# Performance work log

Measured on AMD Instinct MI355X. Metric: run time of the kernel, lower is better.

The kernel has to match this reference:

```python
import jax, jax.numpy as jnp
import numpy as np

F_SIZE = 256
N_HEAD = 4
D_HEAD = F_SIZE // N_HEAD
B = 16384
E = 31  # number of 'other' entities


def setup_inputs() -> dict:
    key = jax.random.key(0)
    ks = jax.random.split(key, 9)
    s = 1.0 / np.sqrt(F_SIZE)  # ~ nn.Linear init scale
    inp = {
        "ego": jax.random.normal(ks[0], (B, 1, F_SIZE), dtype=jnp.float32),
        "others": jax.random.normal(ks[1], (B, E, F_SIZE), dtype=jnp.float32),
        "mask": jax.random.randint(ks[2], (B, E + 1), 0, 2).astype(bool),
        "Wq": jax.random.uniform(ks[3], (F_SIZE, F_SIZE), jnp.float32, -s, s),
        "Wk": jax.random.uniform(ks[4], (F_SIZE, F_SIZE), jnp.float32, -s, s),
        "Wv": jax.random.uniform(ks[5], (F_SIZE, F_SIZE), jnp.float32, -s, s),
        "Wok": jax.random.uniform(ks[6], (F_SIZE, F_SIZE), jnp.float32, -s, s),
        "Wov": jax.random.uniform(ks[7], (F_SIZE, F_SIZE), jnp.float32, -s, s),
        "Wc": jax.random.uniform(ks[8], (F_SIZE, F_SIZE), jnp.float32, -s, s),
    }
    return inp


def reference(ego, others, mask, Wq, Wk, Wv, Wok, Wov, Wc):
    b = others.shape[0]
    e = others.shape[1]
    # nn.Linear(bias=False): y = x @ W.T
    ego_q = (ego @ Wq.T).reshape(b, 1, N_HEAD, D_HEAD)
    ego_k = (ego @ Wk.T).reshape(b, 1, N_HEAD, D_HEAD)
    ego_v = (ego @ Wv.T).reshape(b, 1, N_HEAD, D_HEAD)
    oth_k = (others @ Wok.T).reshape(b, e, N_HEAD, D_HEAD)
    oth_v = (others @ Wov.T).reshape(b, e, N_HEAD, D_HEAD)
    all_k = jnp.concatenate([ego_k, oth_k], axis=1)  # (b, e+1, h, d)
    all_v = jnp.concatenate([ego_v, oth_v], axis=1)
    # scores: single query per head -> (b, h, 1, e+1)
    scores = jnp.einsum('bqhd,bkhd->bhqk', ego_q, all_k) / np.sqrt(D_HEAD)
    scores = jnp.where(mask[:, None, None, :], jnp.float32(-1e9), scores)
    attn = jax.nn.softmax(scores, axis=-1)
    value = jnp.einsum('bhqk,bkhd->bqhd', attn, all_v).reshape(b, F_SIZE)
    res = ((value @ Wc.T) + ego[:, 0, :]) * 0.5
    return res, attn
```

## Files before the change

### kernel.cpp

```cpp
#include <hip/hip_runtime.h>
#include <hip/hip_bf16.h>

typedef __attribute__((ext_vector_type(8))) short bf16x8;
typedef __attribute__((ext_vector_type(4))) float f32x4;

#define NB 16384
#define NE 31

static __device__ __forceinline__ unsigned short f2b(float f) {
  unsigned int u = __builtin_bit_cast(unsigned int, f);
  return (unsigned short)((u + 0x7fffu + ((u >> 16) & 1u)) >> 16);
}
static __device__ __forceinline__ float b2f(unsigned short h) {
  return __builtin_bit_cast(float, ((unsigned int)h) << 16);
}
static __device__ __forceinline__ unsigned int cvtpk(float a, float b) {
  unsigned int r;
  asm("v_cvt_pk_bf16_f32 %0, %1, %2" : "=v"(r) : "v"(a), "v"(b));
  return r;
}
static __device__ __forceinline__ float lo16(unsigned int v) {
  return __builtin_bit_cast(float, v << 16);
}
static __device__ __forceinline__ float hi16(unsigned int v) {
  return __builtin_bit_cast(float, v & 0xffff0000u);
}

__global__ void k0_all(const float* __restrict__ wq, const float* __restrict__ wk,
                       const float* __restrict__ wv, const float* __restrict__ wok,
                       const float* __restrict__ wov, const float* __restrict__ wc,
                       unsigned short* __restrict__ W1, unsigned short* __restrict__ W2) {
  int r = blockIdx.x, k = threadIdx.x;
  if (r < 1024) {
    if (r < 256) {
      W1[r * 256 + k] = f2b(0.125f * wq[r * 256 + k]);
    } else if (r < 512) {
      W1[r * 256 + k] = f2b(wk[(r - 256) * 256 + k]);
    } else if (r < 768) {
      W1[r * 256 + k] = f2b(wv[(r - 512) * 256 + k]);
    } else {
      int n = r - 768;
      W2[n * 1280 + 1024 + k] = f2b(wc[n * 256 + k]);
    }
  } else if (r < 2048) {
    int m = r - 1024;
    int h = m >> 8, c = m & 255;
    float acc = 0.f;
#pragma unroll 8
    for (int d = 0; d < 64; ++d)
      acc = fmaf(wq[(h * 64 + d) * 256 + k], wok[(h * 64 + d) * 256 + c], acc);
    W1[(768 + m) * 256 + k] = f2b(0.125f * acc);
  } else {
    int n = r - 2048;
#pragma unroll 1
    for (int mi = 0; mi < 4; ++mi) {
      float acc = 0.f;
#pragma unroll 8
      for (int d = 0; d < 64; ++d)
        acc = fmaf(wov[(mi * 64 + d) * 256 + k], wc[n * 256 + mi * 64 + d], acc);
      W2[n * 1280 + mi * 256 + k] = f2b(acc);
    }
  }
}

__global__ __launch_bounds__(256, 2)
void k1b(const float* __restrict__ ego, const unsigned short* __restrict__ W1,
         unsigned short* __restrict__ qkv2) {
  __shared__ __align__(16) unsigned short Al[64 * 256];
  const int tid = threadIdx.x;
  const int bM = (blockIdx.x >> 1) * 64;
  const int half = (blockIdx.x & 1) * 896;
#pragma unroll
  for (int it = 0; it < 8; ++it) {
    int c = tid + it * 256;
    int row = c >> 5, k8 = c & 31;
    const float4* g = (const float4*)(ego + (size_t)(bM + row) * 256 + k8 * 8);
    float4 x = g[0], y = g[1];
    float t[8] = {x.x, x.y, x.z, x.w, y.x, y.y, y.z, y.w};
    bf16x8 v;
#pragma unroll
    for (int j = 0; j < 8; ++j) v[j] = (short)f2b(t[j]);
    int byteoff = row * 512 + ((k8 * 16) ^ ((row & 7) << 4));
    *(bf16x8*)((char*)Al + byteoff) = v;
  }
  __syncthreads();
  const int w = tid >> 6, lane = tid & 63, lr = lane & 15, lkg = lane >> 4;
#pragma unroll 1
  for (int cb = 0; cb < 7; ++cb) {
    int bN = half + w * 224 + cb * 32;
    f32x4 acc[4][2];
#pragma unroll
    for (int mt = 0; mt < 4; ++mt)
#pragma unroll
      for (int nt = 0; nt < 2; ++nt) acc[mt][nt] = (f32x4){0.f, 0.f, 0.f, 0.f};
#pragma unroll
    for (int kk = 0; kk < 8; ++kk) {
      int kidx = kk * 32 + lkg * 8;
      bf16x8 bfr[2];
#pragma unroll
      for (int nt = 0; nt < 2; ++nt)
        bfr[nt] = *(const bf16x8*)(W1 + (size_t)(bN + nt * 16 + lr) * 256 + kidx);
#pragma unroll
      for (int mt = 0; mt < 4; ++mt) {
        int row = mt * 16 + lr;
        int byteoff = row * 512 + ((kidx * 2) ^ ((row & 7) << 4));
        bf16x8 a = *(const bf16x8*)((const char*)Al + byteoff);
#pragma unroll
        for (int nt = 0; nt < 2; ++nt)
          acc[mt][nt] = __builtin_amdgcn_mfma_f32_16x16x32_bf16(a, bfr[nt], acc[mt][nt], 0, 0, 0);
      }
    }
#pragma unroll
    for (int mt = 0; mt < 4; ++mt)
#pragma unroll
      for (int nt = 0; nt < 2; ++nt)
#pragma unroll
        for (int j = 0; j < 4; ++j) {
          int row = bM + mt * 16 + lkg * 4 + j;
          int col = bN + nt * 16 + lr;
          qkv2[(size_t)row * 1792 + col] = f2b(acc[mt][nt][j]);
        }
  }
}

__global__ __launch_bounds__(256, 2)
void ks_attn(const float* __restrict__ others, const int* __restrict__ mask,
             const unsigned short* __restrict__ qkv2,
             unsigned short* __restrict__ u,
             float* __restrict__ attnout) {
  __shared__ __align__(16) unsigned short Xs[4][8192];
  __shared__ __align__(16) float Ps[4][32][4];
  const int tid = threadIdx.x;
  const int w = tid >> 6, lane = tid & 63, lr = lane & 15, lkg = lane >> 4;
  const size_t b = (size_t)blockIdx.x * 4 + w;
  char* Xc = (char*)Xs[w];
  float (*P)[4] = Ps[w];
  const unsigned short* qk = qkv2 + b * 1792;

  bf16x8 af[8];
#pragma unroll
  for (int kk = 0; kk < 8; ++kk)
    af[kk] = *(const bf16x8*)(qk + 768 + (lr & 3) * 256 + kk * 32 + lkg * 8);
  ushort4 qa = *(const ushort4*)(qk + lkg * 64 + lr * 4);
  ushort4 kb = *(const ushort4*)(qk + 256 + lkg * 64 + lr * 4);
  ushort4 ve = *(const ushort4*)(qk + 512 + lane * 4);
  int mk0 = mask[b * 32 + 1 + lr];
  int mk1 = (lr == 15) ? 1 : mask[b * 32 + 17 + lr];
  int mkE = mask[b * 32];

  uint2 xv[NE];
  {
    const char* src = (const char*)(others + b * (NE * 256)) + lane * 16;
#pragma unroll
    for (int j = 0; j < NE; ++j) {
      float4 f = *(const float4*)(src + j * 1024);
      uint2 v;
      v.x = cvtpk(f.x, f.y);
      v.y = cvtpk(f.z, f.w);
      xv[j] = v;
      *(uint2*)(Xc + j * 512 + ((lane * 8) ^ ((j & 15) << 4))) = v;
    }
    uint2 z; z.x = 0; z.y = 0;
    *(uint2*)(Xc + 31 * 512 + ((lane * 8) ^ ((31 & 15) << 4))) = z;
  }

  float s0p = b2f(qa.x) * b2f(kb.x) + b2f(qa.y) * b2f(kb.y) +
              b2f(qa.z) * b2f(kb.z) + b2f(qa.w) * b2f(kb.w);
#pragma unroll
  for (int off = 1; off < 16; off <<= 1) s0p += __shfl_xor(s0p, off, 16);
  float s0h[4];
  s0h[0] = __shfl(s0p, 0);
  s0h[1] = __shfl(s0p, 16);
  s0h[2] = __shfl(s0p, 32);
  s0h[3] = __shfl(s0p, 48);

  asm volatile("s_waitcnt lgkmcnt(0)" ::: "memory");
  __builtin_amdgcn_sched_barrier(0);

  f32x4 acc0 = (f32x4){0.f, 0.f, 0.f, 0.f};
  f32x4 acc1 = (f32x4){0.f, 0.f, 0.f, 0.f};
#pragma unroll
  for (int kk = 0; kk < 8; ++kk) {
    int co = kk * 64 + lkg * 16;
    bf16x8 b0 = *(const bf16x8*)(Xc + lr * 512 + (co ^ (lr << 4)));
    bf16x8 b1 = *(const bf16x8*)(Xc + (16 + lr) * 512 + (co ^ (lr << 4)));
    acc0 = __builtin_amdgcn_mfma_f32_16x16x32_bf16(af[kk], b0, acc0, 0, 0, 0);
    acc1 = __builtin_amdgcn_mfma_f32_16x16x32_bf16(af[kk], b1, acc1, 0, 0, 0);
  }

  float pr0[4], pr1[4], p0v[4];
#pragma unroll
  for (int j = 0; j < 4; ++j) {
    float sj0 = mk0 ? -1e9f : acc0[j];
    float sj1 = mk1 ? -1e9f : acc1[j];
    float se  = mkE ? -1e9f : s0h[j];
    float mx = fmaxf(se, fmaxf(sj0, sj1));
#pragma unroll
    for (int off = 1; off < 16; off <<= 1) mx = fmaxf(mx, __shfl_xor(mx, off, 16));
    float e0 = __expf(sj0 - mx), e1 = __expf(sj1 - mx), ee = __expf(se - mx);
    float sm = e0 + e1;
#pragma unroll
    for (int off = 1; off < 16; off <<= 1) sm += __shfl_xor(sm, off, 16);
    float rinv = 1.f / (sm + ee);
    pr0[j] = e0 * rinv;
    pr1[j] = e1 * rinv;
    p0v[j] = ee * rinv;
  }
  if (lkg == 0) {
    float4 q0, q1;
    q0.x = pr0[0]; q0.y = pr0[1]; q0.z = pr0[2]; q0.w = pr0[3];
    *(float4*)&P[1 + lr][0] = q0;
    if (lr < 15) {
      q1.x = pr1[0]; q1.y = pr1[1]; q1.z = pr1[2]; q1.w = pr1[3];
      *(float4*)&P[17 + lr][0] = q1;
    }
    if (lr == 0) {
      float4 qe;
      qe.x = p0v[0]; qe.y = p0v[1]; qe.z = p0v[2]; qe.w = p0v[3];
      *(float4*)&P[0][0] = qe;
    }
#pragma unroll
    for (int j = 0; j < 4; ++j) {
      attnout[b * 128 + j * 32 + 1 + lr] = pr0[j];
      if (lr < 15) attnout[b * 128 + j * 32 + 17 + lr] = pr1[j];
      if (lr == 0) attnout[b * 128 + j * 32] = p0v[j];
    }
  }
  asm volatile("s_waitcnt lgkmcnt(0)" ::: "memory");
  __builtin_amdgcn_sched_barrier(0);

  f32x4 cx[4];
#pragma unroll
  for (int h = 0; h < 4; ++h) cx[h] = (f32x4){0.f, 0.f, 0.f, 0.f};
#pragma unroll
  for (int e = 0; e < NE; ++e) {
    float4 p = *(const float4*)&P[1 + e][0];
    uint2 v = xv[e];
    float x0 = lo16(v.x), x1 = hi16(v.x), x2 = lo16(v.y), x3 = hi16(v.y);
    cx[0][0] = fmaf(p.x, x0, cx[0][0]); cx[0][1] = fmaf(p.x, x1, cx[0][1]);
    cx[0][2] = fmaf(p.x, x2, cx[0][2]); cx[0][3] = fmaf(p.x, x3, cx[0][3]);
    cx[1][0] = fmaf(p.y, x0, cx[1][0]); cx[1][1] = fmaf(p.y, x1, cx[1][1]);
    cx[1][2] = fmaf(p.y, x2, cx[1][2]); cx[1][3] = fmaf(p.y, x3, cx[1][3]);
    cx[2][0] = fmaf(p.z, x0, cx[2][0]); cx[2][1] = fmaf(p.z, x1, cx[2][1]);
    cx[2][2] = fmaf(p.z, x2, cx[2][2]); cx[2][3] = fmaf(p.z, x3, cx[2][3]);
    cx[3][0] = fmaf(p.w, x0, cx[3][0]); cx[3][1] = fmaf(p.w, x1, cx[3][1]);
    cx[3][2] = fmaf(p.w, x2, cx[3][2]); cx[3][3] = fmaf(p.w, x3, cx[3][3]);
  }
#pragma unroll
  for (int h = 0; h < 4; ++h) {
    ushort4 st;
    st.x = f2b(cx[h][0]); st.y = f2b(cx[h][1]);
    st.z = f2b(cx[h][2]); st.w = f2b(cx[h][3]);
    *(ushort4*)(u + b * 1280 + h * 256 + lane * 4) = st;
  }
  float p0h = P[0][lkg];
  ushort4 sv;
  sv.x = f2b(p0h * b2f(ve.x)); sv.y = f2b(p0h * b2f(ve.y));
  sv.z = f2b(p0h * b2f(ve.z)); sv.w = f2b(p0h * b2f(ve.w));
  *(ushort4*)(u + b * 1280 + 1024 + lane * 4) = sv;
}

__global__ __launch_bounds__(256, 2)
void k4_out(const unsigned short* __restrict__ u, const unsigned short* __restrict__ W2,
            const float* __restrict__ ego, float* __restrict__ out) {
  __shared__ __align__(16) unsigned short Au[32 * 256];
  const int tid = threadIdx.x;
  const int bM = blockIdx.x * 32;
  const int w = tid >> 6, lane = tid & 63, lr = lane & 15, lkg = lane >> 4;
  f32x4 acc[2][4];
#pragma unroll
  for (int mt = 0; mt < 2; ++mt)
#pragma unroll
    for (int nt = 0; nt < 4; ++nt) acc[mt][nt] = (f32x4){0.f, 0.f, 0.f, 0.f};
#pragma unroll 1
  for (int kc = 0; kc < 5; ++kc) {
#pragma unroll
    for (int it = 0; it < 4; ++it) {
      int c = tid + it * 256;
      int row = c >> 5, k8 = c & 31;
      bf16x8 v = *(const bf16x8*)(u + (size_t)(bM + row) * 1280 + kc * 256 + k8 * 8);
      int byteoff = row * 512 + ((k8 * 16) ^ ((row & 7) << 4));
      *(bf16x8*)((char*)Au + byteoff) = v;
    }
    __syncthreads();
#pragma unroll
    for (int kk = 0; kk < 8; ++kk) {
      int kidx = kk * 32 + lkg * 8;
      bf16x8 bfr[4];
#pragma unroll
      for (int nt = 0; nt < 4; ++nt)
        bfr[nt] = *(const bf16x8*)(W2 + (size_t)(w * 64 + nt * 16 + lr) * 1280 + kc * 256 + kidx);
#pragma unroll
      for (int mt = 0; mt < 2; ++mt) {
        int row = mt * 16 + lr;
        int byteoff = row * 512 + ((kidx * 2) ^ ((row & 7) << 4));
        bf16x8 a = *(const bf16x8*)((const char*)Au + byteoff);
#pragma unroll
        for (int nt = 0; nt < 4; ++nt)
          acc[mt][nt] = __builtin_amdgcn_mfma_f32_16x16x32_bf16(a, bfr[nt], acc[mt][nt], 0, 0, 0);
      }
    }
    __syncthreads();
  }
#pragma unroll
  for (int mt = 0; mt < 2; ++mt)
#pragma unroll
    for (int nt = 0; nt < 4; ++nt)
#pragma unroll
      for (int j = 0; j < 4; ++j) {
        int row = bM + mt * 16 + lkg * 4 + j;
        int col = w * 64 + nt * 16 + lr;
        out[(size_t)row * 256 + col] = (acc[mt][nt][j] + ego[(size_t)row * 256 + col]) * 0.5f;
      }
}

extern "C" void kernel_launch(void* const* d_in, const int* in_sizes, int n_in,
                              void* d_out, int out_size, void* d_ws, size_t ws_size,
                              hipStream_t stream) {
  const float* ego    = (const float*)d_in[0];
  const float* others = (const float*)d_in[1];
  const int*   mask   = (const int*)d_in[2];
  const float* wq  = (const float*)d_in[3];
  const float* wk  = (const float*)d_in[4];
  const float* wv  = (const float*)d_in[5];
  const float* wok = (const float*)d_in[6];
  const float* wov = (const float*)d_in[7];
  const float* wc  = (const float*)d_in[8];

  unsigned short* W1   = (unsigned short*)d_ws;
  unsigned short* W2   = W1 + 1792 * 256;
  unsigned short* qkv2 = W2 + 256 * 1280;
  unsigned short* u    = qkv2 + (size_t)NB * 1792;

  float* res  = (float*)d_out;
  float* attn = res + (size_t)NB * 256;

  hipLaunchKernelGGL(k0_all, dim3(2304), dim3(256), 0, stream,
                     wq, wk, wv, wok, wov, wc, W1, W2);
  hipLaunchKernelGGL(k1b,    dim3(512),  dim3(256), 0, stream, ego, W1, qkv2);
  hipLaunchKernelGGL(ks_attn, dim3(NB / 4), dim3(256), 0, stream,
                     others, mask, qkv2, u, attn);
  hipLaunchKernelGGL(k4_out, dim3(512),  dim3(256), 0, stream, u, W2, ego, res);
}
```

Measured before the change: 227.4 us.

## Make attention kernel persistent over 8 batches with register prefetch of next inputs

Each wave now processes 8 consecutive batch rows in a loop instead of one. The next row's 'others' tile, q/k/v and mask are loaded into registers while the current row's scores, softmax and weighted sum are computed. The grid shrinks by 8x and launch bounds drop to 1 block per SIMD to make room for the 31 float4 prefetch registers. The aim is to hide global-load latency in this memory-bound kernel, at the cost of lower occupancy and fewer blocks (512) to spread across CUs.

```diff
diff --git a/kernel.cpp b/kernel.cpp
--- a/kernel.cpp
+++ b/kernel.cpp
@@ -123,7 +123,7 @@
   }
 }
 
-__global__ __launch_bounds__(256, 2)
+__global__ __launch_bounds__(256, 1)
 void ks_attn(const float* __restrict__ others, const int* __restrict__ mask,
              const unsigned short* __restrict__ qkv2,
              unsigned short* __restrict__ u,
@@ -132,132 +132,178 @@
   __shared__ __align__(16) float Ps[4][32][4];
   const int tid = threadIdx.x;
   const int w = tid >> 6, lane = tid & 63, lr = lane & 15, lkg = lane >> 4;
-  const size_t b = (size_t)blockIdx.x * 4 + w;
+  const size_t b0 = ((size_t)blockIdx.x * 4 + w) * 8;
   char* Xc = (char*)Xs[w];
   float (*P)[4] = Ps[w];
-  const unsigned short* qk = qkv2 + b * 1792;
-
+
+  float4 pf[NE];
+  uint2 xv[NE];
   bf16x8 af[8];
-#pragma unroll
-  for (int kk = 0; kk < 8; ++kk)
-    af[kk] = *(const bf16x8*)(qk + 768 + (lr & 3) * 256 + kk * 32 + lkg * 8);
-  ushort4 qa = *(const ushort4*)(qk + lkg * 64 + lr * 4);
-  ushort4 kb = *(const ushort4*)(qk + 256 + lkg * 64 + lr * 4);
-  ushort4 ve = *(const ushort4*)(qk + 512 + lane * 4);
-  int mk0 = mask[b * 32 + 1 + lr];
-  int mk1 = (lr == 15) ? 1 : mask[b * 32 + 17 + lr];
-  int mkE = mask[b * 32];
-
-  uint2 xv[NE];
+  ushort4 qa, kb, ve;
+  int mk0, mk1, mkE;
+
   {
-    const char* src = (const char*)(others + b * (NE * 256)) + lane * 16;
+    const char* src = (const char*)(others + b0 * (NE * 256)) + lane * 16;
+#pragma unroll
+    for (int j = 0; j < NE; ++j) pf[j] = *(const float4*)(src + j * 1024);
+    const unsigned short* qk = qkv2 + b0 * 1792;
+#pragma unroll
+    for (int kk = 0; kk < 8; ++kk)
+      af[kk] = *(const bf16x8*)(qk + 768 + (lr & 3) * 256 + kk * 32 + lkg * 8);
+    qa = *(const ushort4*)(qk + lkg * 64 + lr * 4);
+    kb = *(const ushort4*)(qk + 256 + lkg * 64 + lr * 4);
+    ve = *(const ushort4*)(qk + 512 + lane * 4);
+    mk0 = mask[b0 * 32 + 1 + lr];
+    mk1 = (lr == 15) ? 1 : mask[b0 * 32 + 17 + lr];
+    mkE = mask[b0 * 32];
+    uint2 z; z.x = 0; z.y = 0;
+    *(uint2*)(Xc + 31 * 512 + ((lane * 8) ^ ((31 & 15) << 4))) = z;
 #pragma unroll
     for (int j = 0; j < NE; ++j) {
-      float4 f = *(const float4*)(src + j * 1024);
       uint2 v;
-      v.x = cvtpk(f.x, f.y);
-      v.y = cvtpk(f.z, f.w);
+      v.x = cvtpk(pf[j].x, pf[j].y);
+      v.y = cvtpk(pf[j].z, pf[j].w);
       xv[j] = v;
       *(uint2*)(Xc + j * 512 + ((lane * 8) ^ ((j & 15) << 4))) = v;
     }
-    uint2 z; z.x = 0; z.y = 0;
-    *(uint2*)(Xc + 31 * 512 + ((lane * 8) ^ ((31 & 15) << 4))) = z;
-  }
-
-  float s0p = b2f(qa.x) * b2f(kb.x) + b2f(qa.y) * b2f(kb.y) +
-              b2f(qa.z) * b2f(kb.z) + b2f(qa.w) * b2f(kb.w);
-#pragma unroll
-  for (int off = 1; off < 16; off <<= 1) s0p += __shfl_xor(s0p, off, 16);
-  float s0h[4];
-  s0h[0] = __shfl(s0p, 0);
-  s0h[1] = __shfl(s0p, 16);
-  s0h[2] = __shfl(s0p, 32);
-  s0h[3] = __shfl(s0p, 48);
-
-  asm volatile("s_waitcnt lgkmcnt(0)" ::: "memory");
-  __builtin_amdgcn_sched_barrier(0);
-
-  f32x4 acc0 = (f32x4){0.f, 0.f, 0.f, 0.f};
-  f32x4 acc1 = (f32x4){0.f, 0.f, 0.f, 0.f};
-#pragma unroll
-  for (int kk = 0; kk < 8; ++kk) {
-    int co = kk * 64 + lkg * 16;
-    bf16x8 b0 = *(const bf16x8*)(Xc + lr * 512 + (co ^ (lr << 4)));
-    bf16x8 b1 = *(const bf16x8*)(Xc + (16 + lr) * 512 + (co ^ (lr << 4)));
-    acc0 = __builtin_amdgcn_mfma_f32_16x16x32_bf16(af[kk], b0, acc0, 0, 0, 0);
-    acc1 = __builtin_amdgcn_mfma_f32_16x16x32_bf16(af[kk], b1, acc1, 0, 0, 0);
-  }
-
-  float pr0[4], pr1[4], p0v[4];
-#pragma unroll
-  for (int j = 0; j < 4; ++j) {
-    float sj0 = mk0 ? -1e9f : acc0[j];
-    float sj1 = mk1 ? -1e9f : acc1[j];
-    float se  = mkE ? -1e9f : s0h[j];
-    float mx = fmaxf(se, fmaxf(sj0, sj1));
-#pragma unroll
-    for (int off = 1; off < 16; off <<= 1) mx = fmaxf(mx, __shfl_xor(mx, off, 16));
-    float e0 = __expf(sj0 - mx), e1 = __expf(sj1 - mx), ee = __expf(se - mx);
-    float sm = e0 + e1;
-#pragma unroll
-    for (int off = 1; off < 16; off <<= 1) sm += __shfl_xor(sm, off, 16);
-    float rinv = 1.f / (sm + ee);
-    pr0[j] = e0 * rinv;
-    pr1[j] = e1 * rinv;
-    p0v[j] = ee * rinv;
-  }
-  if (lkg == 0) {
-    float4 q0, q1;
-    q0.x = pr0[0]; q0.y = pr0[1]; q0.z = pr0[2]; q0.w = pr0[3];
-    *(float4*)&P[1 + lr][0] = q0;
-    if (lr < 15) {
-      q1.x = pr1[0]; q1.y = pr1[1]; q1.z = pr1[2]; q1.w = pr1[3];
-      *(float4*)&P[17 + lr][0] = q1;
-    }
-    if (lr == 0) {
-      float4 qe;
-      qe.x = p0v[0]; qe.y = p0v[1]; qe.z = p0v[2]; qe.w = p0v[3];
-      *(float4*)&P[0][0] = qe;
-    }
+  }
+
+#pragma unroll 1
+  for (int it = 0; it < 8; ++it) {
+    const size_t b = b0 + it;
+    const size_t bn = b + 1;
+    const bool more = (it < 7);
+
+    if (more) {
+      const char* src = (const char*)(others + bn * (NE * 256)) + lane * 16;
+#pragma unroll
+      for (int j = 0; j < NE; ++j) pf[j] = *(const float4*)(src + j * 1024);
+    }
+    __builtin_amdgcn_sched_barrier(0);
+
+    float s0p = b2f(qa.x) * b2f(kb.x) + b2f(qa.y) * b2f(kb.y) +
+                b2f(qa.z) * b2f(kb.z) + b2f(qa.w) * b2f(kb.w);
+#pragma unroll
+    for (int off = 1; off < 16; off <<= 1) s0p += __shfl_xor(s0p, off, 16);
+    float s0h[4];
+    s0h[0] = __shfl(s0p, 0);
+    s0h[1] = __shfl(s0p, 16);
+    s0h[2] = __shfl(s0p, 32);
+    s0h[3] = __shfl(s0p, 48);
+    if (more) {
+      const unsigned short* qk = qkv2 + bn * 1792;
+      qa = *(const ushort4*)(qk + lkg * 64 + lr * 4);
+      kb = *(const ushort4*)(qk + 256 + lkg * 64 + lr * 4);
+    }
+
+    f32x4 acc0 = (f32x4){0.f, 0.f, 0.f, 0.f};
+    f32x4 acc1 = (f32x4){0.f, 0.f, 0.f, 0.f};
+#pragma unroll
+    for (int kk = 0; kk < 8; ++kk) {
+      int co = kk * 64 + lkg * 16;
+      bf16x8 bf0 = *(const bf16x8*)(Xc + lr * 512 + (co ^ (lr << 4)));
+      bf16x8 bf1 = *(const bf16x8*)(Xc + (16 + lr) * 512 + (co ^ (lr << 4)));
+      acc0 = __builtin_amdgcn_mfma_f32_16x16x32_bf16(af[kk], bf0, acc0, 0, 0, 0);
+      acc1 = __builtin_amdgcn_mfma_f32_16x16x32_bf16(af[kk], bf1, acc1, 0, 0, 0);
+    }
+    if (more) {
+      const unsigned short* qk = qkv2 + bn * 1792;
+#pragma unroll
+      for (int kk = 0; kk < 8; ++kk)
+        af[kk] = *(const bf16x8*)(qk + 768 + (lr & 3) * 256 + kk * 32 + lkg * 8);
+    }
+
+    float pr0[4], pr1[4], p0v[4];
 #pragma unroll
     for (int j = 0; j < 4; ++j) {
-      attnout[b * 128 + j * 32 + 1 + lr] = pr0[j];
-      if (lr < 15) attnout[b * 128 + j * 32 + 17 + lr] = pr1[j];
-      if (lr == 0) attnout[b * 128 + j * 32] = p0v[j];
-    }
-  }
-  asm volatile("s_waitcnt lgkmcnt(0)" ::: "memory");
-  __builtin_amdgcn_sched_barrier(0);
-
-  f32x4 cx[4];
-#pragma unroll
-  for (int h = 0; h < 4; ++h) cx[h] = (f32x4){0.f, 0.f, 0.f, 0.f};
-#pragma unroll
-  for (int e = 0; e < NE; ++e) {
-    float4 p = *(const float4*)&P[1 + e][0];
-    uint2 v = xv[e];
-    float x0 = lo16(v.x), x1 = hi16(v.x), x2 = lo16(v.y), x3 = hi16(v.y);
-    cx[0][0] = fmaf(p.x, x0, cx[0][0]); cx[0][1] = fmaf(p.x, x1, cx[0][1]);
-    cx[0][2] = fmaf(p.x, x2, cx[0][2]); cx[0][3] = fmaf(p.x, x3, cx[0][3]);
-    cx[1][0] = fmaf(p.y, x0, cx[1][0]); cx[1][1] = fmaf(p.y, x1, cx[1][1]);
-    cx[1][2] = fmaf(p.y, x2, cx[1][2]); cx[1][3] = fmaf(p.y, x3, cx[1][3]);
-    cx[2][0] = fmaf(p.z, x0, cx[2][0]); cx[2][1] = fmaf(p.z, x1, cx[2][1]);
-    cx[2][2] = fmaf(p.z, x2, cx[2][2]); cx[2][3] = fmaf(p.z, x3, cx[2][3]);
-    cx[3][0] = fmaf(p.w, x0, cx[3][0]); cx[3][1] = fmaf(p.w, x1, cx[3][1]);
-    cx[3][2] = fmaf(p.w, x2, cx[3][2]); cx[3][3] = fmaf(p.w, x3, cx[3][3]);
-  }
-#pragma unroll
-  for (int h = 0; h < 4; ++h) {
-    ushort4 st;
-    st.x = f2b(cx[h][0]); st.y = f2b(cx[h][1]);
-    st.z = f2b(cx[h][2]); st.w = f2b(cx[h][3]);
-    *(ushort4*)(u + b * 1280 + h * 256 + lane * 4) = st;
-  }
-  float p0h = P[0][lkg];
-  ushort4 sv;
-  sv.x = f2b(p0h * b2f(ve.x)); sv.y = f2b(p0h * b2f(ve.y));
-  sv.z = f2b(p0h * b2f(ve.z)); sv.w = f2b(p0h * b2f(ve.w));
-  *(ushort4*)(u + b * 1280 + 1024 + lane * 4) = sv;
+      float sj0 = mk0 ? -1e9f : acc0[j];
+      float sj1 = mk1 ? -1e9f : acc1[j];
+      float se  = mkE ? -1e9f : s0h[j];
+      float mx = fmaxf(se, fmaxf(sj0, sj1));
+#pragma unroll
+      for (int off = 1; off < 16; off <<= 1) mx = fmaxf(mx, __shfl_xor(mx, off, 16));
+      float e0 = __expf(sj0 - mx), e1 = __expf(sj1 - mx), ee = __expf(se - mx);
+      float sm = e0 + e1;
+#pragma unroll
+      for (int off = 1; off < 16; off <<= 1) sm += __shfl_xor(sm, off, 16);
+      float rinv = 1.f / (sm + ee);
+      pr0[j] = e0 * rinv;
+      pr1[j] = e1 * rinv;
+      p0v[j] = ee * rinv;
+    }
+    if (more) {
+      mk0 = mask[bn * 32 + 1 + lr];
+      mk1 = (lr == 15) ? 1 : mask[bn * 32 + 17 + lr];
+      mkE = mask[bn * 32];
+    }
+    if (lkg == 0) {
+      float4 q0, q1;
+      q0.x = pr0[0]; q0.y = pr0[1]; q0.z = pr0[2]; q0.w = pr0[3];
+      *(float4*)&P[1 + lr][0] = q0;
+      if (lr < 15) {
+        q1.x = pr1[0]; q1.y = pr1[1]; q1.z = pr1[2]; q1.w = pr1[3];
+        *(float4*)&P[17 + lr][0] = q1;
+      }
+      if (lr == 0) {
+        float4 qe;
+        qe.x = p0v[0]; qe.y = p0v[1]; qe.z = p0v[2]; qe.w = p0v[3];
+        *(float4*)&P[0][0] = qe;
+      }
+#pragma unroll
+      for (int j = 0; j < 4; ++j) {
+        attnout[b * 128 + j * 32 + 1 + lr] = pr0[j];
+        if (lr < 15) attnout[b * 128 + j * 32 + 17 + lr] = pr1[j];
+        if (lr == 0) attnout[b * 128 + j * 32] = p0v[j];
+      }
+    }
+    asm volatile("s_waitcnt lgkmcnt(0)" ::: "memory");
+    __builtin_amdgcn_sched_barrier(0);
+
+    f32x4 cx[4];
+#pragma unroll
+    for (int h = 0; h < 4; ++h) cx[h] = (f32x4){0.f, 0.f, 0.f, 0.f};
+#pragma unroll
+    for (int e = 0; e < NE; ++e) {
+      float4 p = *(const float4*)&P[1 + e][0];
+      uint2 v = xv[e];
+      float x0 = lo16(v.x), x1 = hi16(v.x), x2 = lo16(v.y), x3 = hi16(v.y);
+      cx[0][0] = fmaf(p.x, x0, cx[0][0]); cx[0][1] = fmaf(p.x, x1, cx[0][1]);
+      cx[0][2] = fmaf(p.x, x2, cx[0][2]); cx[0][3] = fmaf(p.x, x3, cx[0][3]);
+      cx[1][0] = fmaf(p.y, x0, cx[1][0]); cx[1][1] = fmaf(p.y, x1, cx[1][1]);
+      cx[1][2] = fmaf(p.y, x2, cx[1][2]); cx[1][3] = fmaf(p.y, x3, cx[1][3]);
+      cx[2][0] = fmaf(p.z, x0, cx[2][0]); cx[2][1] = fmaf(p.z, x1, cx[2][1]);
+      cx[2][2] = fmaf(p.z, x2, cx[2][2]); cx[2][3] = fmaf(p.z, x3, cx[2][3]);
+      cx[3][0] = fmaf(p.w, x0, cx[3][0]); cx[3][1] = fmaf(p.w, x1, cx[3][1]);
+      cx[3][2] = fmaf(p.w, x2, cx[3][2]); cx[3][3] = fmaf(p.w, x3, cx[3][3]);
+    }
+#pragma unroll
+    for (int h = 0; h < 4; ++h) {
+      ushort4 st;
+      st.x = f2b(cx[h][0]); st.y = f2b(cx[h][1]);
+      st.z = f2b(cx[h][2]); st.w = f2b(cx[h][3]);
+      *(ushort4*)(u + b * 1280 + h * 256 + lane * 4) = st;
+    }
+    {
+      float p0h = P[0][lkg];
+      ushort4 sv;
+      sv.x = f2b(p0h * b2f(ve.x)); sv.y = f2b(p0h * b2f(ve.y));
+      sv.z = f2b(p0h * b2f(ve.z)); sv.w = f2b(p0h * b2f(ve.w));
+      *(ushort4*)(u + b * 1280 + 1024 + lane * 4) = sv;
+    }
+    if (more) ve = *(const ushort4*)(qkv2 + bn * 1792 + 512 + lane * 4);
+
+    if (more) {
+#pragma unroll
+      for (int j = 0; j < NE; ++j) {
+        uint2 v;
+        v.x = cvtpk(pf[j].x, pf[j].y);
+        v.y = cvtpk(pf[j].z, pf[j].w);
+        xv[j] = v;
+        *(uint2*)(Xc + j * 512 + ((lane * 8) ^ ((j & 15) << 4))) = v;
+      }
+    }
+    __builtin_amdgcn_sched_barrier(0);
+  }
 }
 
 __global__ __launch_bounds__(256, 2)
@@ -338,7 +384,7 @@
   hipLaunchKernelGGL(k0_all, dim3(2304), dim3(256), 0, stream,
                      wq, wk, wv, wok, wov, wc, W1, W2);
   hipLaunchKernelGGL(k1b,    dim3(512),  dim3(256), 0, stream, ego, W1, qkv2);
-  hipLaunchKernelGGL(ks_attn, dim3(NB / 4), dim3(256), 0, stream,
+  hipLaunchKernelGGL(ks_attn, dim3(NB / 32), dim3(256), 0, stream,
                      others, mask, qkv2, u, attn);
   hipLaunchKernelGGL(k4_out, dim3(512),  dim3(256), 0, stream, u, W2, ego, res);
 }
```

Result: slower. 247.2 us (+8.7%).

## Hoist A fragments into registers in k1b and restage k4_out with 16-row tiles

Applied to the files above, without the earlier changes.

In k1b the ego tile is converted with packed bf16 conversion instructions, and the A-operand fragments are loaded from LDS once into registers and reused across all seven column blocks instead of being reloaded each time. In k4_out the block now covers 16 rows and stages the full 1280-wide K row in LDS up front, removing the per-chunk barriers. The grid doubles to 1024 blocks for more parallelism. The cost is much higher register pressure in k1b (32 bf16x8 fragments) and twice as many W2 reads from global/L2 in k4_out.

```diff
diff --git a/kernel.cpp b/kernel.cpp
--- a/kernel.cpp
+++ b/kernel.cpp
@@ -76,15 +76,28 @@
     int row = c >> 5, k8 = c & 31;
     const float4* g = (const float4*)(ego + (size_t)(bM + row) * 256 + k8 * 8);
     float4 x = g[0], y = g[1];
-    float t[8] = {x.x, x.y, x.z, x.w, y.x, y.y, y.z, y.w};
-    bf16x8 v;
-#pragma unroll
-    for (int j = 0; j < 8; ++j) v[j] = (short)f2b(t[j]);
+    uint2 v0, v1;
+    v0.x = cvtpk(x.x, x.y); v0.y = cvtpk(x.z, x.w);
+    v1.x = cvtpk(y.x, y.y); v1.y = cvtpk(y.z, y.w);
     int byteoff = row * 512 + ((k8 * 16) ^ ((row & 7) << 4));
-    *(bf16x8*)((char*)Al + byteoff) = v;
+    *(uint2*)((char*)Al + byteoff) = v0;
+    *(uint2*)((char*)Al + byteoff + 8) = v1;
   }
   __syncthreads();
   const int w = tid >> 6, lane = tid & 63, lr = lane & 15, lkg = lane >> 4;
+
+  bf16x8 af[4][8];
+#pragma unroll
+  for (int mt = 0; mt < 4; ++mt) {
+    int row = mt * 16 + lr;
+#pragma unroll
+    for (int kk = 0; kk < 8; ++kk) {
+      int kidx = kk * 32 + lkg * 8;
+      int byteoff = row * 512 + ((kidx * 2) ^ ((row & 7) << 4));
+      af[mt][kk] = *(const bf16x8*)((const char*)Al + byteoff);
+    }
+  }
+
 #pragma unroll 1
   for (int cb = 0; cb < 7; ++cb) {
     int bN = half + w * 224 + cb * 32;
@@ -101,14 +114,10 @@
       for (int nt = 0; nt < 2; ++nt)
         bfr[nt] = *(const bf16x8*)(W1 + (size_t)(bN + nt * 16 + lr) * 256 + kidx);
 #pragma unroll
-      for (int mt = 0; mt < 4; ++mt) {
-        int row = mt * 16 + lr;
-        int byteoff = row * 512 + ((kidx * 2) ^ ((row & 7) << 4));
-        bf16x8 a = *(const bf16x8*)((const char*)Al + byteoff);
+      for (int mt = 0; mt < 4; ++mt)
 #pragma unroll
         for (int nt = 0; nt < 2; ++nt)
-          acc[mt][nt] = __builtin_amdgcn_mfma_f32_16x16x32_bf16(a, bfr[nt], acc[mt][nt], 0, 0, 0);
-      }
+          acc[mt][nt] = __builtin_amdgcn_mfma_f32_16x16x32_bf16(af[mt][kk], bfr[nt], acc[mt][nt], 0, 0, 0);
     }
 #pragma unroll
     for (int mt = 0; mt < 4; ++mt)
@@ -263,55 +272,46 @@
 __global__ __launch_bounds__(256, 2)
 void k4_out(const unsigned short* __restrict__ u, const unsigned short* __restrict__ W2,
             const float* __restrict__ ego, float* __restrict__ out) {
-  __shared__ __align__(16) unsigned short Au[32 * 256];
+  __shared__ __align__(16) unsigned short Au[16 * 1280];
   const int tid = threadIdx.x;
-  const int bM = blockIdx.x * 32;
+  const int bM = blockIdx.x * 16;
   const int w = tid >> 6, lane = tid & 63, lr = lane & 15, lkg = lane >> 4;
-  f32x4 acc[2][4];
-#pragma unroll
-  for (int mt = 0; mt < 2; ++mt)
-#pragma unroll
-    for (int nt = 0; nt < 4; ++nt) acc[mt][nt] = (f32x4){0.f, 0.f, 0.f, 0.f};
+#pragma unroll
+  for (int it = 0; it < 10; ++it) {
+    int c = tid + it * 256;
+    int row = c / 160, k8 = c - row * 160;
+    bf16x8 v = *(const bf16x8*)(u + (size_t)(bM + row) * 1280 + k8 * 8);
+    int byteoff = row * 2560 + ((k8 * 16) ^ ((row & 7) << 4));
+    *(bf16x8*)((char*)Au + byteoff) = v;
+  }
+  __syncthreads();
+  f32x4 acc[4];
+#pragma unroll
+  for (int nt = 0; nt < 4; ++nt) acc[nt] = (f32x4){0.f, 0.f, 0.f, 0.f};
 #pragma unroll 1
   for (int kc = 0; kc < 5; ++kc) {
 #pragma unroll
-    for (int it = 0; it < 4; ++it) {
-      int c = tid + it * 256;
-      int row = c >> 5, k8 = c & 31;
-      bf16x8 v = *(const bf16x8*)(u + (size_t)(bM + row) * 1280 + kc * 256 + k8 * 8);
-      int byteoff = row * 512 + ((k8 * 16) ^ ((row & 7) << 4));
-      *(bf16x8*)((char*)Au + byteoff) = v;
-    }
-    __syncthreads();
-#pragma unroll
     for (int kk = 0; kk < 8; ++kk) {
-      int kidx = kk * 32 + lkg * 8;
+      int kidx = kc * 256 + kk * 32 + lkg * 8;
       bf16x8 bfr[4];
 #pragma unroll
       for (int nt = 0; nt < 4; ++nt)
-        bfr[nt] = *(const bf16x8*)(W2 + (size_t)(w * 64 + nt * 16 + lr) * 1280 + kc * 256 + kidx);
-#pragma unroll
-      for (int mt = 0; mt < 2; ++mt) {
-        int row = mt * 16 + lr;
-        int byteoff = row * 512 + ((kidx * 2) ^ ((row & 7) << 4));
-        bf16x8 a = *(const bf16x8*)((const char*)Au + byteoff);
-#pragma unroll
-        for (int nt = 0; nt < 4; ++nt)
-          acc[mt][nt] = __builtin_amdgcn_mfma_f32_16x16x32_bf16(a, bfr[nt], acc[mt][nt], 0, 0, 0);
-      }
-    }
-    __syncthreads();
-  }
-#pragma unroll
-  for (int mt = 0; mt < 2; ++mt)
-#pragma unroll
-    for (int nt = 0; nt < 4; ++nt)
-#pragma unroll
-      for (int j = 0; j < 4; ++j) {
-        int row = bM + mt * 16 + lkg * 4 + j;
-        int col = w * 64 + nt * 16 + lr;
-        out[(size_t)row * 256 + col] = (acc[mt][nt][j] + ego[(size_t)row * 256 + col]) * 0.5f;
-      }
+        bfr[nt] = *(const bf16x8*)(W2 + (size_t)(w * 64 + nt * 16 + lr) * 1280 + kidx);
+      int byteoff = lr * 2560 + ((kidx * 2) ^ ((lr & 7) << 4));
+      bf16x8 a = *(const bf16x8*)((const char*)Au + byteoff);
+#pragma unroll
+      for (int nt = 0; nt < 4; ++nt)
+        acc[nt] = __builtin_amdgcn_mfma_f32_16x16x32_bf16(a, bfr[nt], acc[nt], 0, 0, 0);
+    }
+  }
+#pragma unroll
+  for (int nt = 0; nt < 4; ++nt)
+#pragma unroll
+    for (int j = 0; j < 4; ++j) {
+      int row = bM + lkg * 4 + j;
+      int col = w * 64 + nt * 16 + lr;
+      out[(size_t)row * 256 + col] = (acc[nt][j] + ego[(size_t)row * 256 + col]) * 0.5f;
+    }
 }
 
 extern "C" void kernel_launch(void* const* d_in, const int* in_sizes, int n_in,
@@ -340,5 +340,5 @@
   hipLaunchKernelGGL(k1b,    dim3(512),  dim3(256), 0, stream, ego, W1, qkv2);
   hipLaunchKernelGGL(ks_attn, dim3(NB / 4), dim3(256), 0, stream,
                      others, mask, qkv2, u, attn);
-  hipLaunchKernelGGL(k4_out, dim3(512),  dim3(256), 0, stream, u, W2, ego, res);
-}
+  hipLaunchKernelGGL(k4_out, dim3(1024), dim3(256), 0, stream, u, W2, ego, res);
+}
```

After: 264.4 us. +16.3%, slower.

## Run attention kernel as one-wave blocks and drop register-held others copy

Applied to the files above, without the earlier changes.

The attention kernel now launches one 64-thread block per batch row instead of four waves per block. It also stops keeping the 31-entry bf16 copy of 'others' in registers and rereads it from LDS during the weighted sum. Attention probabilities are broadcast with cross-lane shuffles instead of going through a shared P buffer. The aim is lower register pressure and higher occupancy so more global loads of 'others' are in flight. The cost is extra LDS reads and shuffle traffic, plus four times as many small blocks to schedule.

```diff
diff --git a/kernel.cpp b/kernel.cpp
--- a/kernel.cpp
+++ b/kernel.cpp
@@ -18,12 +18,6 @@
   unsigned int r;
   asm("v_cvt_pk_bf16_f32 %0, %1, %2" : "=v"(r) : "v"(a), "v"(b));
   return r;
-}
-static __device__ __forceinline__ float lo16(unsigned int v) {
-  return __builtin_bit_cast(float, v << 16);
-}
-static __device__ __forceinline__ float hi16(unsigned int v) {
-  return __builtin_bit_cast(float, v & 0xffff0000u);
 }
 
 __global__ void k0_all(const float* __restrict__ wq, const float* __restrict__ wk,
@@ -123,18 +117,16 @@
   }
 }
 
-__global__ __launch_bounds__(256, 2)
+__global__ __launch_bounds__(64, 4)
 void ks_attn(const float* __restrict__ others, const int* __restrict__ mask,
              const unsigned short* __restrict__ qkv2,
              unsigned short* __restrict__ u,
              float* __restrict__ attnout) {
-  __shared__ __align__(16) unsigned short Xs[4][8192];
-  __shared__ __align__(16) float Ps[4][32][4];
-  const int tid = threadIdx.x;
-  const int w = tid >> 6, lane = tid & 63, lr = lane & 15, lkg = lane >> 4;
-  const size_t b = (size_t)blockIdx.x * 4 + w;
-  char* Xc = (char*)Xs[w];
-  float (*P)[4] = Ps[w];
+  __shared__ __align__(16) unsigned short Xs[8192];
+  const int lane = threadIdx.x;
+  const int lr = lane & 15, lkg = lane >> 4;
+  const size_t b = blockIdx.x;
+  char* Xc = (char*)Xs;
   const unsigned short* qk = qkv2 + b * 1792;
 
   bf16x8 af[8];
@@ -148,7 +140,6 @@
   int mk1 = (lr == 15) ? 1 : mask[b * 32 + 17 + lr];
   int mkE = mask[b * 32];
 
-  uint2 xv[NE];
   {
     const char* src = (const char*)(others + b * (NE * 256)) + lane * 16;
 #pragma unroll
@@ -157,7 +148,6 @@
       uint2 v;
       v.x = cvtpk(f.x, f.y);
       v.y = cvtpk(f.z, f.w);
-      xv[j] = v;
       *(uint2*)(Xc + j * 512 + ((lane * 8) ^ ((j & 15) << 4))) = v;
     }
     uint2 z; z.x = 0; z.y = 0;
@@ -207,18 +197,6 @@
     p0v[j] = ee * rinv;
   }
   if (lkg == 0) {
-    float4 q0, q1;
-    q0.x = pr0[0]; q0.y = pr0[1]; q0.z = pr0[2]; q0.w = pr0[3];
-    *(float4*)&P[1 + lr][0] = q0;
-    if (lr < 15) {
-      q1.x = pr1[0]; q1.y = pr1[1]; q1.z = pr1[2]; q1.w = pr1[3];
-      *(float4*)&P[17 + lr][0] = q1;
-    }
-    if (lr == 0) {
-      float4 qe;
-      qe.x = p0v[0]; qe.y = p0v[1]; qe.z = p0v[2]; qe.w = p0v[3];
-      *(float4*)&P[0][0] = qe;
-    }
 #pragma unroll
     for (int j = 0; j < 4; ++j) {
       attnout[b * 128 + j * 32 + 1 + lr] = pr0[j];
@@ -226,25 +204,30 @@
       if (lr == 0) attnout[b * 128 + j * 32] = p0v[j];
     }
   }
-  asm volatile("s_waitcnt lgkmcnt(0)" ::: "memory");
-  __builtin_amdgcn_sched_barrier(0);
 
   f32x4 cx[4];
 #pragma unroll
   for (int h = 0; h < 4; ++h) cx[h] = (f32x4){0.f, 0.f, 0.f, 0.f};
 #pragma unroll
   for (int e = 0; e < NE; ++e) {
-    float4 p = *(const float4*)&P[1 + e][0];
-    uint2 v = xv[e];
-    float x0 = lo16(v.x), x1 = hi16(v.x), x2 = lo16(v.y), x3 = hi16(v.y);
-    cx[0][0] = fmaf(p.x, x0, cx[0][0]); cx[0][1] = fmaf(p.x, x1, cx[0][1]);
-    cx[0][2] = fmaf(p.x, x2, cx[0][2]); cx[0][3] = fmaf(p.x, x3, cx[0][3]);
-    cx[1][0] = fmaf(p.y, x0, cx[1][0]); cx[1][1] = fmaf(p.y, x1, cx[1][1]);
-    cx[1][2] = fmaf(p.y, x2, cx[1][2]); cx[1][3] = fmaf(p.y, x3, cx[1][3]);
-    cx[2][0] = fmaf(p.z, x0, cx[2][0]); cx[2][1] = fmaf(p.z, x1, cx[2][1]);
-    cx[2][2] = fmaf(p.z, x2, cx[2][2]); cx[2][3] = fmaf(p.z, x3, cx[2][3]);
-    cx[3][0] = fmaf(p.w, x0, cx[3][0]); cx[3][1] = fmaf(p.w, x1, cx[3][1]);
-    cx[3][2] = fmaf(p.w, x2, cx[3][2]); cx[3][3] = fmaf(p.w, x3, cx[3][3]);
+    float p0, p1, p2, p3;
+    if (e < 16) {
+      p0 = __shfl(pr0[0], e); p1 = __shfl(pr0[1], e);
+      p2 = __shfl(pr0[2], e); p3 = __shfl(pr0[3], e);
+    } else {
+      p0 = __shfl(pr1[0], e - 16); p1 = __shfl(pr1[1], e - 16);
+      p2 = __shfl(pr1[2], e - 16); p3 = __shfl(pr1[3], e - 16);
+    }
+    ushort4 xr = *(const ushort4*)(Xc + e * 512 + ((lane * 8) ^ ((e & 15) << 4)));
+    float x0 = b2f(xr.x), x1 = b2f(xr.y), x2 = b2f(xr.z), x3 = b2f(xr.w);
+    cx[0][0] = fmaf(p0, x0, cx[0][0]); cx[0][1] = fmaf(p0, x1, cx[0][1]);
+    cx[0][2] = fmaf(p0, x2, cx[0][2]); cx[0][3] = fmaf(p0, x3, cx[0][3]);
+    cx[1][0] = fmaf(p1, x0, cx[1][0]); cx[1][1] = fmaf(p1, x1, cx[1][1]);
+    cx[1][2] = fmaf(p1, x2, cx[1][2]); cx[1][3] = fmaf(p1, x3, cx[1][3]);
+    cx[2][0] = fmaf(p2, x0, cx[2][0]); cx[2][1] = fmaf(p2, x1, cx[2][1]);
+    cx[2][2] = fmaf(p2, x2, cx[2][2]); cx[2][3] = fmaf(p2, x3, cx[2][3]);
+    cx[3][0] = fmaf(p3, x0, cx[3][0]); cx[3][1] = fmaf(p3, x1, cx[3][1]);
+    cx[3][2] = fmaf(p3, x2, cx[3][2]); cx[3][3] = fmaf(p3, x3, cx[3][3]);
   }
 #pragma unroll
   for (int h = 0; h < 4; ++h) {
@@ -253,11 +236,13 @@
     st.z = f2b(cx[h][2]); st.w = f2b(cx[h][3]);
     *(ushort4*)(u + b * 1280 + h * 256 + lane * 4) = st;
   }
-  float p0h = P[0][lkg];
-  ushort4 sv;
-  sv.x = f2b(p0h * b2f(ve.x)); sv.y = f2b(p0h * b2f(ve.y));
-  sv.z = f2b(p0h * b2f(ve.z)); sv.w = f2b(p0h * b2f(ve.w));
-  *(ushort4*)(u + b * 1280 + 1024 + lane * 4) = sv;
+  {
+    float p0h = (lkg == 0) ? p0v[0] : (lkg == 1) ? p0v[1] : (lkg == 2) ? p0v[2] : p0v[3];
+    ushort4 sv;
+    sv.x = f2b(p0h * b2f(ve.x)); sv.y = f2b(p0h * b2f(ve.y));
+    sv.z = f2b(p0h * b2f(ve.z)); sv.w = f2b(p0h * b2f(ve.w));
+    *(ushort4*)(u + b * 1280 + 1024 + lane * 4) = sv;
+  }
 }
 
 __global__ __launch_bounds__(256, 2)
@@ -338,7 +323,7 @@
   hipLaunchKernelGGL(k0_all, dim3(2304), dim3(256), 0, stream,
                      wq, wk, wv, wok, wov, wc, W1, W2);
   hipLaunchKernelGGL(k1b,    dim3(512),  dim3(256), 0, stream, ego, W1, qkv2);
-  hipLaunchKernelGGL(ks_attn, dim3(NB / 4), dim3(256), 0, stream,
+  hipLaunchKernelGGL(ks_attn, dim3(NB), dim3(64), 0, stream,
                      others, mask, qkv2, u, attn);
   hipLaunchKernelGGL(k4_out, dim3(512),  dim3(256), 0, stream, u, W2, ego, res);
 }
```

Result: no change. 229.9 us (+1.1%).
